# Kernel tuning notes

Measured on AMD Instinct MI355X. Metric: run time of the kernel, lower is better.

## Reference

```python
import jax, jax.numpy as jnp
import numpy as np


def setup_inputs() -> dict:
    key = jax.random.key(0)
    ks = jax.random.split(key, 8)
    B, L, D, N, DM = 2, 2048, 2048, 8, 1024
    return {
        "x": jax.random.normal(ks[0], (B, L, D), jnp.float32),
        "A_log": jax.random.normal(ks[1], (D, N), jnp.float32),
        "x_proj_w": jax.random.normal(ks[2], (2 * N, D), jnp.float32) * (D ** -0.5),
        "x_proj_b": jax.random.normal(ks[3], (2 * N,), jnp.float32) * 0.02,
        "dt_proj_w": jax.random.normal(ks[4], (D, D), jnp.float32) * (D ** -0.5),
        "dt_proj_b": jax.random.normal(ks[5], (D,), jnp.float32) * 0.02,
        "out_proj_w": jax.random.normal(ks[6], (DM, D), jnp.float32) * (D ** -0.5),
        "out_proj_b": jax.random.normal(ks[7], (DM,), jnp.float32) * 0.02,
    }


def reference(x, A_log, x_proj_w, x_proj_b, dt_proj_w, dt_proj_b, out_proj_w, out_proj_b):
    # x: (B, L, D);  A_log: (D, N)
    A = -jnp.exp(A_log)                                   # (D, N), negative -> stable decay
    x_dbl = x @ x_proj_w.T + x_proj_b                     # (B, L, 2N): per-token B_t, C_t
    Bm, Cm = jnp.split(x_dbl, 2, axis=-1)                 # each (B, L, N)
    dt = jax.nn.softplus(x @ dt_proj_w.T + dt_proj_b)     # (B, L, D) selective timestep

    Bsz, L, D = x.shape
    N = A_log.shape[1]

    def step(h, inp):
        dt_t, B_t, C_t, x_t = inp                         # (B,D),(B,N),(B,N),(B,D)
        dA = jnp.exp(dt_t[..., None] * A)                 # (B, D, N)
        dB = dt_t[..., None] * B_t[:, None, :]            # (B, D, N)
        h = dA * h + dB * x_t[..., None]                  # (B, D, N)
        y = jnp.einsum("bdn,bn->bd", h, C_t)              # (B, D)
        return h, y

    h0 = jnp.zeros((Bsz, D, N), x.dtype)
    xs = (dt.transpose(1, 0, 2), Bm.transpose(1, 0, 2),
          Cm.transpose(1, 0, 2), x.transpose(1, 0, 2))
    _, ys = jax.lax.scan(step, h0, xs)                    # ys: (L, B, D)
    y = ys.transpose(1, 0, 2)                             # (B, L, D)
    return y @ out_proj_w.T + out_proj_b                  # (B, L, d_model)
```

## Files before the change

### kernel.cpp

```cpp
#include <hip/hip_runtime.h>
#include <hip/hip_bf16.h>

constexpr int Bsz = 2;
constexpr int L   = 2048;
constexpr int D   = 2048;
constexpr int Nst = 8;
constexpr int DM  = 1024;
constexpr int M   = Bsz * L;

constexpr int CH  = 64;
constexpr int T   = L / CH;
constexpr int BDN = Bsz * D * Nst;

typedef __bf16 bf16x8 __attribute__((ext_vector_type(8)));
typedef float f32x4  __attribute__((ext_vector_type(4)));

__global__ void cvt2_f32_bf16(const float* __restrict__ a, __bf16* __restrict__ oa, int n4a,
                              const float* __restrict__ b, __bf16* __restrict__ ob, int n4b) {
    int i = blockIdx.x * blockDim.x + threadIdx.x;
    const float* src; __bf16* dst; int j;
    if (i < n4a)            { src = a; dst = oa; j = i; }
    else if (i < n4a + n4b) { src = b; dst = ob; j = i - n4a; }
    else return;
    float4 v = reinterpret_cast<const float4*>(src)[j];
    union { __bf16 bb[4]; ushort4 u; } cv;
    cv.bb[0] = (__bf16)v.x; cv.bb[1] = (__bf16)v.y; cv.bb[2] = (__bf16)v.z; cv.bb[3] = (__bf16)v.w;
    reinterpret_cast<ushort4*>(dst)[j] = cv.u;
}

__global__ __launch_bounds__(256) void xdbl_kernel(
    const float* __restrict__ x, const float* __restrict__ w,
    const float* __restrict__ bias, float* __restrict__ xdbl,
    __bf16* __restrict__ x_bf)
{
    __shared__ float sw[16 * 2048];
    const int tid = threadIdx.x;
    for (int i = tid; i < 16 * 2048 / 4; i += 256)
        reinterpret_cast<float4*>(sw)[i] = reinterpret_cast<const float4*>(w)[i];
    __syncthreads();

    const int lane = tid & 63;
    const int wrow = tid >> 6;
    for (int rr = 0; rr < 4; ++rr) {
        const int row = blockIdx.x * 16 + wrow * 4 + rr;
        const float* xr = x + (size_t)row * D;
        __bf16* xb = x_bf + (size_t)row * D;
        float acc[16];
#pragma unroll
        for (int j = 0; j < 16; ++j) acc[j] = 0.f;
        for (int k = lane * 4; k < D; k += 256) {
            float4 xv = *reinterpret_cast<const float4*>(&xr[k]);
            union { __bf16 b[4]; ushort4 u; } cv;
            cv.b[0] = (__bf16)xv.x; cv.b[1] = (__bf16)xv.y;
            cv.b[2] = (__bf16)xv.z; cv.b[3] = (__bf16)xv.w;
            *reinterpret_cast<ushort4*>(&xb[k]) = cv.u;
#pragma unroll
            for (int j = 0; j < 16; ++j) {
                float4 wv = *reinterpret_cast<const float4*>(&sw[j * D + k]);
                acc[j] += xv.x * wv.x + xv.y * wv.y + xv.z * wv.z + xv.w * wv.w;
            }
        }
#pragma unroll
        for (int j = 0; j < 16; ++j) {
            float v = acc[j];
#pragma unroll
            for (int off = 32; off > 0; off >>= 1) v += __shfl_down(v, off, 64);
            if (lane == 0) xdbl[(size_t)row * 16 + j] = v + bias[j];
        }
    }
}

__device__ inline void async16(__bf16* lds, const __bf16* g) {
    __builtin_amdgcn_global_load_lds(
        (const __attribute__((address_space(1))) void*)g,
        (__attribute__((address_space(3))) void*)lds, 16, 0, 0);
}

template <int MODE, int SWZ>
__global__ __launch_bounds__(512, 4) void gemm_bt(
    const __bf16* __restrict__ A, const __bf16* __restrict__ Bw,
    const float* __restrict__ bias, void* __restrict__ Cout,
    int N, int Kfull, int Ksub)
{
    constexpr int BM = 128, BN = 128, BK = 64;
    const int NT = Ksub / BK;
    const int zoff = blockIdx.z * Ksub;
    __shared__ __attribute__((aligned(16))) __bf16 lds[2][2][BM * BK];

    int bx = blockIdx.x, by = blockIdx.y;
    if (SWZ) {
        const int lin = by * gridDim.x + bx;
        const int cpx = (gridDim.x * gridDim.y) >> 3;
        const int swz = (lin & 7) * cpx + (lin >> 3);
        bx = swz % gridDim.x; by = swz / gridDim.x;
    }

    const int tid  = threadIdx.x;
    const int lane = tid & 63;
    const int wid  = tid >> 6;
    const int wm   = wid >> 2, wn = wid & 3;
    const int rowBase = by * BM;
    const int colBase = bx * BN;
    const int lrow = lane & 15;
    const int kgrp = lane >> 4;

    float bv[2] = {0.f, 0.f};
    if (MODE != 3) {
#pragma unroll
        for (int n = 0; n < 2; ++n)
            bv[n] = bias[colBase + wn * 32 + n * 16 + lrow];
    }
    asm volatile("s_waitcnt vmcnt(0)" ::: "memory");

    const int trow = tid >> 3;
    const int scol = ((tid & 7) ^ (trow & 7)) * 8;
    const __bf16* gA[2]; const __bf16* gB[2];
#pragma unroll
    for (int ro = 0; ro < 2; ++ro) {
        gA[ro] = A  + (size_t)(rowBase + ro * 64 + trow) * Kfull + zoff + scol;
        gB[ro] = Bw + (size_t)(colBase + ro * 64 + trow) * Kfull + zoff + scol;
    }

    f32x4 acc[4][2];
#pragma unroll
    for (int i = 0; i < 4; ++i)
#pragma unroll
        for (int j = 0; j < 2; ++j) acc[i][j] = f32x4{0.f, 0.f, 0.f, 0.f};

    auto stage = [&](int kt, int bsel) {
        const int k0 = kt * BK;
#pragma unroll
        for (int ro = 0; ro < 2; ++ro) {
            async16(&lds[bsel][0][ro * 4096 + tid * 8], gA[ro] + k0);
            async16(&lds[bsel][1][ro * 4096 + tid * 8], gB[ro] + k0);
        }
    };

    stage(0, 0);
    stage(1, 1);

    for (int t = 0; t < NT; ++t) {
        if (t == NT - 1) asm volatile("s_waitcnt vmcnt(0)" ::: "memory");
        else             asm volatile("s_waitcnt vmcnt(4)" ::: "memory");
        __builtin_amdgcn_s_barrier();

        const int cur = t & 1;
        bf16x8 af[4][2], bfr[2][2];
#pragma unroll
        for (int m = 0; m < 4; ++m) {
            const int row = wm * 64 + m * 16 + lrow;
#pragma unroll
            for (int kk = 0; kk < 2; ++kk) {
                const int slot = (kk * 4 + kgrp) ^ (lrow & 7);
                af[m][kk] = *reinterpret_cast<const bf16x8*>(&lds[cur][0][row * 64 + slot * 8]);
            }
        }
#pragma unroll
        for (int n = 0; n < 2; ++n) {
            const int row = wn * 32 + n * 16 + lrow;
#pragma unroll
            for (int kk = 0; kk < 2; ++kk) {
                const int slot = (kk * 4 + kgrp) ^ (lrow & 7);
                bfr[n][kk] = *reinterpret_cast<const bf16x8*>(&lds[cur][1][row * 64 + slot * 8]);
            }
        }
        asm volatile("s_waitcnt lgkmcnt(0)" ::: "memory");
        __builtin_amdgcn_s_barrier();

        if (t + 2 < NT) stage(t + 2, cur);

        __builtin_amdgcn_s_setprio(1);
#pragma unroll
        for (int kk = 0; kk < 2; ++kk)
#pragma unroll
            for (int m = 0; m < 4; ++m)
#pragma unroll
                for (int n = 0; n < 2; ++n)
                    acc[m][n] = __builtin_amdgcn_mfma_f32_16x16x32_bf16(af[m][kk], bfr[n][kk], acc[m][n], 0, 0, 0);
        __builtin_amdgcn_s_setprio(0);
    }

#pragma unroll
    for (int m = 0; m < 4; ++m) {
        const int row = rowBase + wm * 64 + m * 16 + kgrp * 4;
#pragma unroll
        for (int n = 0; n < 2; ++n) {
            const int col = colBase + wn * 32 + n * 16 + lrow;
#pragma unroll
            for (int r = 0; r < 4; ++r) {
                float v = acc[m][n][r] + bv[n];
                if (MODE == 1) {
                    v = (v > 20.f) ? v : log1pf(expf(v));
                    ((__bf16*)Cout)[(size_t)(row + r) * N + col] = (__bf16)v;
                } else {
                    ((float*)Cout)[(size_t)blockIdx.z * M * N + (size_t)(row + r) * N + col] = v;
                }
            }
        }
    }
}

__global__ __launch_bounds__(256) void reduce_bias(
    const float* __restrict__ part, const float* __restrict__ bias,
    float* __restrict__ out)
{
    const int i = blockIdx.x * blockDim.x + threadIdx.x;
    const int n4 = M * DM / 4;
    if (i >= n4) return;
    float4 a = reinterpret_cast<const float4*>(part)[i];
    float4 b = reinterpret_cast<const float4*>(part + (size_t)M * DM)[i];
    float4 bb = *reinterpret_cast<const float4*>(&bias[(i * 4) % DM]);
    float4 r;
    r.x = a.x + b.x + bb.x; r.y = a.y + b.y + bb.y;
    r.z = a.z + b.z + bb.z; r.w = a.w + b.w + bb.w;
    reinterpret_cast<float4*>(out)[i] = r;
}

__global__ __launch_bounds__(64) void scan_p1(
    const __bf16* __restrict__ dt, const __bf16* __restrict__ x,
    const float* __restrict__ xdbl, const float* __restrict__ A_log,
    float* __restrict__ P, float* __restrict__ Hloc)
{
    const int tid = threadIdx.x;
    int blk = blockIdx.x;
    const int c  = blk % CH;  blk /= CH;
    const int dg = blk % (D / 64);
    const int b  = blk / (D / 64);
    const int d  = dg * 64 + tid;

    float A[Nst], h[Nst], p[Nst];
#pragma unroll
    for (int n = 0; n < Nst; ++n) {
        A[n] = -expf(A_log[(size_t)d * Nst + n]);
        h[n] = 0.f; p[n] = 1.f;
    }

    __shared__ __attribute__((aligned(16))) float sBC[T * 16];
    const float4* src = reinterpret_cast<const float4*>(xdbl + ((size_t)b * L + c * T) * 16);
#pragma unroll
    for (int i = tid; i < T * 4; i += 64)
        reinterpret_cast<float4*>(sBC)[i] = src[i];
    __syncthreads();

    const __bf16* dt_p = dt + ((size_t)b * L + c * T) * D + d;
    const __bf16* x_p  = x  + ((size_t)b * L + c * T) * D + d;
#pragma unroll 4
    for (int t2 = 0; t2 < T; ++t2) {
        const float dtv = (float)dt_p[(size_t)t2 * D];
        const float xv  = (float)x_p[(size_t)t2 * D];
        const float dtx = dtv * xv;
        const float* bc = &sBC[t2 * 16];
#pragma unroll
        for (int n = 0; n < Nst; ++n) {
            const float dA = __expf(dtv * A[n]);
            p[n] *= dA;
            h[n] = dA * h[n] + dtx * bc[n];
        }
    }
    const size_t base = ((size_t)c * Bsz * D + (size_t)b * D + d) * Nst;
#pragma unroll
    for (int n = 0; n < Nst; ++n) { P[base + n] = p[n]; Hloc[base + n] = h[n]; }
}

__global__ __launch_bounds__(256) void scan_p2(
    const float* __restrict__ P, const float* __restrict__ Hloc,
    float* __restrict__ Hstart)
{
    const int id = blockIdx.x * blockDim.x + threadIdx.x;
    if (id >= BDN) return;
    float h = 0.f;
    for (int c = 0; c < CH; ++c) {
        const size_t o = (size_t)c * BDN + id;
        Hstart[o] = h;
        h = P[o] * h + Hloc[o];
    }
}

__global__ __launch_bounds__(64) void scan_p3(
    const __bf16* __restrict__ dt, const __bf16* __restrict__ x,
    const float* __restrict__ xdbl, const float* __restrict__ A_log,
    const float* __restrict__ Hstart, __bf16* __restrict__ y_bf)
{
    const int tid = threadIdx.x;
    int blk = blockIdx.x;
    const int c  = blk % CH;  blk /= CH;
    const int dg = blk % (D / 64);
    const int b  = blk / (D / 64);
    const int d  = dg * 64 + tid;

    float A[Nst], h[Nst];
    const size_t hbase = ((size_t)c * Bsz * D + (size_t)b * D + d) * Nst;
#pragma unroll
    for (int n = 0; n < Nst; ++n) {
        A[n] = -expf(A_log[(size_t)d * Nst + n]);
        h[n] = Hstart[hbase + n];
    }

    __shared__ __attribute__((aligned(16))) float sBC[T * 16];
    const float4* src = reinterpret_cast<const float4*>(xdbl + ((size_t)b * L + c * T) * 16);
#pragma unroll
    for (int i = tid; i < T * 4; i += 64)
        reinterpret_cast<float4*>(sBC)[i] = src[i];
    __syncthreads();

    const __bf16* dt_p = dt + ((size_t)b * L + c * T) * D + d;
    const __bf16* x_p  = x  + ((size_t)b * L + c * T) * D + d;
    __bf16*       y_p  = y_bf + ((size_t)b * L + c * T) * D + d;
#pragma unroll 4
    for (int t2 = 0; t2 < T; ++t2) {
        const float dtv = (float)dt_p[(size_t)t2 * D];
        const float xv  = (float)x_p[(size_t)t2 * D];
        const float dtx = dtv * xv;
        const float* bc = &sBC[t2 * 16];
        float y = 0.f;
#pragma unroll
        for (int n = 0; n < Nst; ++n) {
            const float dA = __expf(dtv * A[n]);
            h[n] = dA * h[n] + dtx * bc[n];
            y = fmaf(h[n], bc[8 + n], y);
        }
        y_p[(size_t)t2 * D] = (__bf16)y;
    }
}

extern "C" void kernel_launch(void* const* d_in, const int* in_sizes, int n_in,
                              void* d_out, int out_size, void* d_ws, size_t ws_size,
                              hipStream_t stream) {
    const float* x     = (const float*)d_in[0];
    const float* A_log = (const float*)d_in[1];
    const float* xpw   = (const float*)d_in[2];
    const float* xpb   = (const float*)d_in[3];
    const float* dtw   = (const float*)d_in[4];
    const float* dtb   = (const float*)d_in[5];
    const float* ow    = (const float*)d_in[6];
    const float* ob    = (const float*)d_in[7];
    float* out = (float*)d_out;

    char* ws = (char*)d_ws;
    __bf16* x_bf    = (__bf16*)(ws);
    __bf16* dtw_bf  = (__bf16*)(ws + 16777216);
    __bf16* ow_bf   = (__bf16*)(ws + 25165824);
    float*  xdbl    = (float* )(ws + 29360128);
    __bf16* dtbuf   = (__bf16*)(ws + 29622272);
    __bf16* y_bf    = (__bf16*)(ws + 63176704);
    float*  P       = (float*)(ws + 16777216);
    float*  Hloc    = (float*)(ws + 46399488);
    float*  Hstart  = (float*)(ws + 54788096);
    float*  Cpart   = (float*)(ws + 29622272);

    const int n4a = D * D / 4, n4b = DM * D / 4;
    cvt2_f32_bf16<<<(n4a + n4b + 255) / 256, 256, 0, stream>>>(dtw, dtw_bf, n4a, ow, ow_bf, n4b);

    xdbl_kernel<<<M / 16, 256, 0, stream>>>(x, xpw, xpb, xdbl, x_bf);

    gemm_bt<1, 1><<<dim3(D / 128, M / 128, 1), 512, 0, stream>>>(x_bf, dtw_bf, dtb, dtbuf, D, D, D);

    const int scan_blocks = Bsz * (D / 64) * CH;
    scan_p1<<<scan_blocks, 64, 0, stream>>>(dtbuf, x_bf, xdbl, A_log, P, Hloc);
    scan_p2<<<(BDN + 255) / 256, 256, 0, stream>>>(P, Hloc, Hstart);
    scan_p3<<<scan_blocks, 64, 0, stream>>>(dtbuf, x_bf, xdbl, A_log, Hstart, y_bf);

    gemm_bt<3, 1><<<dim3(DM / 128, M / 128, 2), 512, 0, stream>>>(y_bf, ow_bf, ob, Cpart, DM, D, D / 2);
    reduce_bias<<<(M * DM / 4 + 255) / 256, 256, 0, stream>>>(Cpart, ob, out);
}
```

Before: 195.8 us.

## Simplify GEMM prefetch to single-ahead and keep dt in fp32

The GEMM main loop is reworked from a two-deep prefetch with split barriers to a single-ahead double buffer. Each iteration now ends with a full vmcnt(0) wait and a barrier. The softplus dt output is stored as fp32 instead of bf16, and both scan passes read it as fp32. The scan scratch buffers P and Hloc move into the output buffer, and Hstart moves into the dt-weight region to fit the larger dt buffer. The changes double dt traffic in the scans and reduce load/compute overlap in the GEMM, trading speed for dt precision and a simpler schedule.

```diff
diff --git a/kernel.cpp b/kernel.cpp
--- a/kernel.cpp
+++ b/kernel.cpp
@@ -79,7 +79,7 @@
 template <int MODE, int SWZ>
 __global__ __launch_bounds__(512, 4) void gemm_bt(
     const __bf16* __restrict__ A, const __bf16* __restrict__ Bw,
-    const float* __restrict__ bias, void* __restrict__ Cout,
+    const float* __restrict__ bias, float* __restrict__ C,
     int N, int Kfull, int Ksub)
 {
     constexpr int BM = 128, BN = 128, BK = 64;
@@ -110,7 +110,6 @@
         for (int n = 0; n < 2; ++n)
             bv[n] = bias[colBase + wn * 32 + n * 16 + lrow];
     }
-    asm volatile("s_waitcnt vmcnt(0)" ::: "memory");
 
     const int trow = tid >> 3;
     const int scol = ((tid & 7) ^ (trow & 7)) * 8;
@@ -137,14 +136,13 @@
     };
 
     stage(0, 0);
-    stage(1, 1);
-
+    asm volatile("s_waitcnt vmcnt(0)" ::: "memory");
+    __builtin_amdgcn_s_barrier();
+
+    int cur = 0;
     for (int t = 0; t < NT; ++t) {
-        if (t == NT - 1) asm volatile("s_waitcnt vmcnt(0)" ::: "memory");
-        else             asm volatile("s_waitcnt vmcnt(4)" ::: "memory");
-        __builtin_amdgcn_s_barrier();
-
-        const int cur = t & 1;
+        if (t + 1 < NT) stage(t + 1, cur ^ 1);
+
         bf16x8 af[4][2], bfr[2][2];
 #pragma unroll
         for (int m = 0; m < 4; ++m) {
@@ -165,9 +163,6 @@
             }
         }
         asm volatile("s_waitcnt lgkmcnt(0)" ::: "memory");
-        __builtin_amdgcn_s_barrier();
-
-        if (t + 2 < NT) stage(t + 2, cur);
 
         __builtin_amdgcn_s_setprio(1);
 #pragma unroll
@@ -178,6 +173,10 @@
                 for (int n = 0; n < 2; ++n)
                     acc[m][n] = __builtin_amdgcn_mfma_f32_16x16x32_bf16(af[m][kk], bfr[n][kk], acc[m][n], 0, 0, 0);
         __builtin_amdgcn_s_setprio(0);
+
+        asm volatile("s_waitcnt vmcnt(0)" ::: "memory");
+        __builtin_amdgcn_s_barrier();
+        cur ^= 1;
     }
 
 #pragma unroll
@@ -191,9 +190,9 @@
                 float v = acc[m][n][r] + bv[n];
                 if (MODE == 1) {
                     v = (v > 20.f) ? v : log1pf(expf(v));
-                    ((__bf16*)Cout)[(size_t)(row + r) * N + col] = (__bf16)v;
+                    C[(size_t)(row + r) * N + col] = v;
                 } else {
-                    ((float*)Cout)[(size_t)blockIdx.z * M * N + (size_t)(row + r) * N + col] = v;
+                    C[(size_t)blockIdx.z * M * N + (size_t)(row + r) * N + col] = v;
                 }
             }
         }
@@ -217,7 +216,7 @@
 }
 
 __global__ __launch_bounds__(64) void scan_p1(
-    const __bf16* __restrict__ dt, const __bf16* __restrict__ x,
+    const float* __restrict__ dt, const __bf16* __restrict__ x,
     const float* __restrict__ xdbl, const float* __restrict__ A_log,
     float* __restrict__ P, float* __restrict__ Hloc)
 {
@@ -242,11 +241,11 @@
         reinterpret_cast<float4*>(sBC)[i] = src[i];
     __syncthreads();
 
-    const __bf16* dt_p = dt + ((size_t)b * L + c * T) * D + d;
+    const float*  dt_p = dt + ((size_t)b * L + c * T) * D + d;
     const __bf16* x_p  = x  + ((size_t)b * L + c * T) * D + d;
 #pragma unroll 4
     for (int t2 = 0; t2 < T; ++t2) {
-        const float dtv = (float)dt_p[(size_t)t2 * D];
+        const float dtv = dt_p[(size_t)t2 * D];
         const float xv  = (float)x_p[(size_t)t2 * D];
         const float dtx = dtv * xv;
         const float* bc = &sBC[t2 * 16];
@@ -277,7 +276,7 @@
 }
 
 __global__ __launch_bounds__(64) void scan_p3(
-    const __bf16* __restrict__ dt, const __bf16* __restrict__ x,
+    const float* __restrict__ dt, const __bf16* __restrict__ x,
     const float* __restrict__ xdbl, const float* __restrict__ A_log,
     const float* __restrict__ Hstart, __bf16* __restrict__ y_bf)
 {
@@ -303,12 +302,12 @@
         reinterpret_cast<float4*>(sBC)[i] = src[i];
     __syncthreads();
 
-    const __bf16* dt_p = dt + ((size_t)b * L + c * T) * D + d;
+    const float*  dt_p = dt + ((size_t)b * L + c * T) * D + d;
     const __bf16* x_p  = x  + ((size_t)b * L + c * T) * D + d;
     __bf16*       y_p  = y_bf + ((size_t)b * L + c * T) * D + d;
 #pragma unroll 4
     for (int t2 = 0; t2 < T; ++t2) {
-        const float dtv = (float)dt_p[(size_t)t2 * D];
+        const float dtv = dt_p[(size_t)t2 * D];
         const float xv  = (float)x_p[(size_t)t2 * D];
         const float dtx = dtv * xv;
         const float* bc = &sBC[t2 * 16];
@@ -341,11 +340,11 @@
     __bf16* dtw_bf  = (__bf16*)(ws + 16777216);
     __bf16* ow_bf   = (__bf16*)(ws + 25165824);
     float*  xdbl    = (float* )(ws + 29360128);
-    __bf16* dtbuf   = (__bf16*)(ws + 29622272);
+    float*  dtbuf   = (float* )(ws + 29622272);
     __bf16* y_bf    = (__bf16*)(ws + 63176704);
-    float*  P       = (float*)(ws + 16777216);
-    float*  Hloc    = (float*)(ws + 46399488);
-    float*  Hstart  = (float*)(ws + 54788096);
+    float*  P       = (float*)d_out;
+    float*  Hloc    = (float*)d_out + (1 << 21);
+    float*  Hstart  = (float*)(ws + 16777216);
     float*  Cpart   = (float*)(ws + 29622272);
 
     const int n4a = D * D / 4, n4b = DM * D / 4;
```

Measured after the change: 186.3 us. 4.8% less time.
